# Kernel tuning notes

Hardware: AMD Instinct MI355X
Metric: run time of the kernel (lower is better)

Reference implementation:

```python
import jax, jax.numpy as jnp
import numpy as np

B, S, D = 2, 2048, 2048
H, KV, DK = 16, 4, 128
G = H // KV  # GQA groups
EPS = 1e-6
BASE = 10000.0


def _rope_tables(seq_len, dim):
    inv_freq = 1.0 / (BASE ** (jnp.arange(0, dim, 2, dtype=jnp.float32) / dim))
    t = jnp.arange(seq_len, dtype=jnp.float32)
    freqs = t[:, None] * inv_freq[None, :]            # [S, dim/2]
    emb = jnp.concatenate([freqs, freqs], axis=-1)    # [S, dim]
    # broadcast over [b, s, h, d]
    return jnp.cos(emb)[None, :, None, :], jnp.sin(emb)[None, :, None, :]


def _rotate_half(x):
    x1, x2 = jnp.split(x, 2, axis=-1)
    return jnp.concatenate([-x2, x1], axis=-1)


def _rms_norm(x, w):
    return x * jax.lax.rsqrt(jnp.mean(x * x, axis=-1, keepdims=True) + EPS) * w


def setup_inputs() -> dict:
    key = jax.random.key(0)
    ks = jax.random.split(key, 5)
    std = 0.02
    return {
        "x": jax.random.normal(ks[0], (B, S, D), jnp.float32),
        "Wq": jax.random.normal(ks[1], (D, H * DK), jnp.float32) * std,
        "Wk": jax.random.normal(ks[2], (D, KV * DK), jnp.float32) * std,
        "Wv": jax.random.normal(ks[3], (D, KV * DK), jnp.float32) * std,
        "Wo": jax.random.normal(ks[4], (H * DK, D), jnp.float32) * std,
        "q_norm_w": jnp.ones((DK,), jnp.float32),
        "k_norm_w": jnp.ones((DK,), jnp.float32),
    }


def reference(x, Wq, Wk, Wv, Wo, q_norm_w, k_norm_w):
    b, s, d = x.shape
    q = (x @ Wq).reshape(b, s, H, DK)
    k = (x @ Wk).reshape(b, s, KV, DK)
    v = (x @ Wv).reshape(b, s, KV, DK)

    # per-head RMSNorm on q/k
    q = _rms_norm(q, q_norm_w)
    k = _rms_norm(k, k_norm_w)

    # RoPE (applied in [b, s, h, d] layout like the original)
    cos, sin = _rope_tables(s, DK)
    q = q * cos + _rotate_half(q) * sin
    k = k * cos + _rotate_half(k) * sin

    # GQA attention without materializing repeated K/V:
    # q: [b, kv, g, s, d];  k, v: [b, kv, s, d]
    q = q.transpose(0, 2, 1, 3).reshape(b, KV, G, s, DK)
    k = k.transpose(0, 2, 1, 3)
    v = v.transpose(0, 2, 1, 3)

    scale = 1.0 / np.sqrt(DK)
    scores = jnp.einsum('bkgqd,bkpd->bkgqp', q, k) * scale  # [b,kv,g,s,s]
    causal = jnp.tril(jnp.ones((s, s), dtype=bool))
    scores = jnp.where(causal, scores, jnp.finfo(scores.dtype).min)
    attn = jax.nn.softmax(scores, axis=-1)
    out = jnp.einsum('bkgqp,bkpd->bkgqd', attn, v)           # [b,kv,g,s,d]

    out = out.reshape(b, H, s, DK).transpose(0, 2, 1, 3).reshape(b, s, H * DK)
    return out @ Wo
```

## Files before the change

### kernel.cpp

```cpp
#include <hip/hip_runtime.h>

typedef __attribute__((ext_vector_type(4))) float f32x4;
typedef __attribute__((ext_vector_type(8))) short s16x8;

struct alignas(8) us4 { ushort x, y, z, w; };

__device__ __forceinline__ ushort f2bf(float f) {
  unsigned u = __builtin_bit_cast(unsigned, f);
  u += 0x7fffu + ((u >> 16) & 1u);
  return (ushort)(u >> 16);
}
__device__ __forceinline__ float bf2f(ushort h) {
  unsigned u = ((unsigned)h) << 16;
  return __builtin_bit_cast(float, u);
}

__device__ __forceinline__ void gload_lds16(const ushort* g, ushort* l) {
  __builtin_amdgcn_global_load_lds((const __attribute__((address_space(1))) unsigned int*)g,
                                   (__attribute__((address_space(3))) unsigned int*)l, 16, 0, 0);
}

__global__ __launch_bounds__(256) void cast_bf16_kernel(const float* __restrict__ in,
                                                        ushort* __restrict__ out, int n4) {
  int i = blockIdx.x * 256 + threadIdx.x;
  int stride = gridDim.x * 256;
  for (; i < n4; i += stride) {
    float4 v = reinterpret_cast<const float4*>(in)[i];
    us4 o;
    o.x = f2bf(v.x); o.y = f2bf(v.y); o.z = f2bf(v.z); o.w = f2bf(v.w);
    reinterpret_cast<us4*>(out)[i] = o;
  }
}

__global__ __launch_bounds__(256) void cast_transpose_kernel(const float* __restrict__ in,
                                                             ushort* __restrict__ out,
                                                             int R, int C) {
  __shared__ float tile[32][33];
  int tx = threadIdx.x & 31, ty = threadIdx.x >> 5;
  int c0 = blockIdx.x * 32, r0 = blockIdx.y * 32;
#pragma unroll
  for (int i = 0; i < 4; ++i)
    tile[ty + i * 8][tx] = in[(size_t)(r0 + ty + i * 8) * C + c0 + tx];
  __syncthreads();
#pragma unroll
  for (int i = 0; i < 4; ++i)
    out[(size_t)(c0 + ty + i * 8) * R + r0 + tx] = f2bf(tile[tx][ty + i * 8]);
}

__global__ void rope_table_kernel(float* __restrict__ rc, float* __restrict__ rs) {
  int t = blockIdx.x, j = threadIdx.x;
  float inv = expf(-(float)j * (9.210340371976184f / 64.0f));
  float ang = (float)t * inv;
  float s, c;
  sincosf(ang, &s, &c);
  rc[t * 64 + j] = c;
  rs[t * 64 + j] = s;
}

__global__ __launch_bounds__(256) void norm_rope_kernel(
    const ushort* __restrict__ qkv, const float* __restrict__ w,
    ushort* __restrict__ out, const float* __restrict__ rc, const float* __restrict__ rs,
    int nheads, int col_off, int out_stride, float oscale) {
  int wv = threadIdx.x >> 6, lane = threadIdx.x & 63;
  int row = blockIdx.x * 4 + wv;
  int token = row / nheads, head = row % nheads;
  int t = token & 2047;
  const ushort* p = qkv + (size_t)token * 3072 + col_off + head * 128;
  float x1 = bf2f(p[lane]), x2 = bf2f(p[lane + 64]);
  float ss = x1 * x1 + x2 * x2;
#pragma unroll
  for (int m = 32; m > 0; m >>= 1) ss += __shfl_xor(ss, m);
  float r = rsqrtf(ss * (1.0f / 128.0f) + 1e-6f);
  float xn1 = x1 * r * w[lane], xn2 = x2 * r * w[lane + 64];
  float c = rc[t * 64 + lane], s = rs[t * 64 + lane];
  ushort* o = out + (size_t)token * out_stride + head * 128;
  o[lane] = f2bf((xn1 * c - xn2 * s) * oscale);
  o[lane + 64] = f2bf((xn2 * c + xn1 * s) * oscale);
}

__global__ __launch_bounds__(256) void v_transpose_kernel(const ushort* __restrict__ qkv,
                                                          ushort* __restrict__ vt) {
  __shared__ ushort tile[64][136];
  int bx = blockIdx.x;
  int st = bx & 31, kvh = (bx >> 5) & 3, b = bx >> 7;
  int s0 = st * 64;
  int tid = threadIdx.x;
#pragma unroll
  for (int p = 0; p < 4; ++p) {
    int idx = p * 2048 + tid * 8;
    int s = idx >> 7, d = idx & 127;
    *(s16x8*)&tile[s][d] =
        *(const s16x8*)&qkv[(size_t)(b * 2048 + s0 + s) * 3072 + 2560 + kvh * 128 + d];
  }
  __syncthreads();
#pragma unroll
  for (int p = 0; p < 4; ++p) {
    int idx = p * 2048 + tid * 8;
    int d = idx >> 6, s = idx & 63;
    s16x8 v;
#pragma unroll
    for (int u = 0; u < 8; ++u) v[u] = (short)tile[s + u][d];
    *(s16x8*)&vt[(size_t)((b * 4 + kvh) * 128 + d) * 2048 + s0 + s] = v;
  }
}

template <bool OUTF32>
__global__ __launch_bounds__(512, 2) void gemm256_kernel(const ushort* __restrict__ A,
                                                         const ushort* __restrict__ Bt,
                                                         void* __restrict__ Cp,
                                                         int M, int N, int K) {
  __shared__ ushort As[3][256][64];
  __shared__ ushort Bs[3][128][64];
  int tid = threadIdx.x;
  int lane = tid & 63, wv = tid >> 6;
  int wm = wv >> 1, wn = wv & 1;
  int lr = lane & 15, lg = lane >> 4;
  int nwg = gridDim.x * gridDim.y;
  int flat = blockIdx.y * gridDim.x + blockIdx.x;
  int swz = (flat & 7) * (nwg >> 3) + (flat >> 3);
  int bx = swz % gridDim.x, by = swz / gridDim.x;
  int m0 = by * 256, n0 = bx * 128;
  int srow8 = lane >> 3;
  int gcol = ((lane & 7) * 8) ^ (srow8 << 3);
  int nt = K >> 6;

  const ushort* Abase = A + (size_t)m0 * K;
  const ushort* Bbase = Bt + (size_t)n0 * K;

  auto stageA = [&](int slot, int t, int p) {
    int r0 = (wv * 4 + p) * 8;
    gload_lds16(&Abase[(size_t)(r0 + srow8) * K + t * 64 + gcol], &As[slot][r0][0]);
  };
  auto stageB = [&](int slot, int t, int p) {
    int r0 = (wv * 2 + p) * 8;
    gload_lds16(&Bbase[(size_t)(r0 + srow8) * K + t * 64 + gcol], &Bs[slot][r0][0]);
  };

  stageA(0, 0, 0); stageA(0, 0, 1); stageB(0, 0, 0);
  stageA(0, 0, 2); stageA(0, 0, 3); stageB(0, 0, 1);
  stageA(1, 1, 0); stageA(1, 1, 1); stageB(1, 1, 0);
  stageA(1, 1, 2); stageA(1, 1, 3); stageB(1, 1, 1);

  f32x4 acc[4][4] = {};
  int arow[4], brow[4], aswz[4], bswz[4];
#pragma unroll
  for (int i = 0; i < 4; ++i) {
    arow[i] = wm * 64 + i * 16 + lr;
    aswz[i] = (arow[i] & 7) << 3;
    brow[i] = wn * 64 + i * 16 + lr;
    bswz[i] = (brow[i] & 7) << 3;
  }

  for (int t = 0; t < nt; ++t) {
    int cur = t % 3, pf = (t + 2) % 3;
    if (t + 1 < nt) {
      asm volatile("s_waitcnt vmcnt(6)" ::: "memory");
    } else {
      asm volatile("s_waitcnt vmcnt(0)" ::: "memory");
    }
    __builtin_amdgcn_s_barrier();
    bool do_pf = (t + 2) < nt;
    {
      s16x8 a[4], b[4];
#pragma unroll
      for (int i = 0; i < 4; ++i) a[i] = *(const s16x8*)&As[cur][arow[i]][(lg * 8) ^ aswz[i]];
#pragma unroll
      for (int j = 0; j < 4; ++j) b[j] = *(const s16x8*)&Bs[cur][brow[j]][(lg * 8) ^ bswz[j]];
      if (do_pf) { stageA(pf, t + 2, 0); stageA(pf, t + 2, 1); stageB(pf, t + 2, 0); }
      __builtin_amdgcn_s_setprio(1);
#pragma unroll
      for (int i = 0; i < 4; ++i)
#pragma unroll
        for (int j = 0; j < 4; ++j)
          acc[i][j] = __builtin_amdgcn_mfma_f32_16x16x32_bf16(a[i], b[j], acc[i][j], 0, 0, 0);
      __builtin_amdgcn_s_setprio(0);
    }
    {
      s16x8 a[4], b[4];
#pragma unroll
      for (int i = 0; i < 4; ++i) a[i] = *(const s16x8*)&As[cur][arow[i]][(32 + lg * 8) ^ aswz[i]];
#pragma unroll
      for (int j = 0; j < 4; ++j) b[j] = *(const s16x8*)&Bs[cur][brow[j]][(32 + lg * 8) ^ bswz[j]];
      if (do_pf) { stageA(pf, t + 2, 2); stageA(pf, t + 2, 3); stageB(pf, t + 2, 1); }
      __builtin_amdgcn_s_setprio(1);
#pragma unroll
      for (int i = 0; i < 4; ++i)
#pragma unroll
        for (int j = 0; j < 4; ++j)
          acc[i][j] = __builtin_amdgcn_mfma_f32_16x16x32_bf16(a[i], b[j], acc[i][j], 0, 0, 0);
      __builtin_amdgcn_s_setprio(0);
    }
  }
#pragma unroll
  for (int i = 0; i < 4; ++i)
#pragma unroll
    for (int j = 0; j < 4; ++j) {
      int row = m0 + wm * 64 + i * 16 + lg * 4;
      int col = n0 + wn * 64 + j * 16 + lr;
#pragma unroll
      for (int r = 0; r < 4; ++r) {
        float v = acc[i][j][r];
        if (OUTF32)
          reinterpret_cast<float*>(Cp)[(size_t)(row + r) * N + col] = v;
        else
          reinterpret_cast<ushort*>(Cp)[(size_t)(row + r) * N + col] = f2bf(v);
      }
    }
}

__global__ __launch_bounds__(256, 2) void attn_kernel(const ushort* __restrict__ Q,
                                                      const ushort* __restrict__ Kn,
                                                      const ushort* __restrict__ Vt,
                                                      ushort* __restrict__ AO) {
  __shared__ ushort Ks[2][64][128];
  __shared__ ushort Vs[2][128][64];
  __shared__ ushort Ps[4][32][64];
  int bx = blockIdx.x;
  int g = bx >> 5, bh = bx & 31;
  int qt = (g < 8) ? (15 - g) : (g - 8);
  int b = bh >> 4, h = bh & 15, kvh = h >> 2;
  int q0 = qt * 128;
  int nt = 2 * qt + 2;
  int tid = threadIdx.x, lane = tid & 63, w = tid >> 6;
  int lr = lane & 15, lg = lane >> 4;

  int ksrow = lane >> 4;
  int kscol = (lane & 15) * 8;
  int vsrow = lane >> 3;
  int vscol = (lane & 7) * 8;

  auto stage = [&](int c, int t) {
    int p0 = t * 64;
#pragma unroll
    for (int p = 0; p < 4; ++p) {
      int r0 = w * 16 + p * 4;
      int row = r0 + ksrow;
      int gc = kscol ^ ((row & 7) << 3);
      gload_lds16(&Kn[(size_t)(b * 2048 + p0 + row) * 512 + kvh * 128 + gc], &Ks[c][r0][0]);
    }
#pragma unroll
    for (int p = 0; p < 4; ++p) {
      int r0 = w * 32 + p * 8;
      int row = r0 + vsrow;
      int gc = vscol ^ ((row & 7) << 3);
      gload_lds16(&Vt[(size_t)((b * 4 + kvh) * 128 + row) * 2048 + p0 + gc], &Vs[c][r0][0]);
    }
  };

  stage(0, 0);

  s16x8 qf[2][4];
#pragma unroll
  for (int qa = 0; qa < 2; ++qa) {
    const ushort* qp = &Q[(size_t)(b * 2048 + q0 + w * 32 + qa * 16 + lr) * 2048 + h * 128];
#pragma unroll
    for (int ks = 0; ks < 4; ++ks) qf[qa][ks] = *(const s16x8*)&qp[ks * 32 + lg * 8];
  }

  f32x4 O[2][8] = {};
  float mrow[2] = {-1e30f, -1e30f};
  float lrow[2] = {0.f, 0.f};

  for (int t = 0; t < nt; ++t) {
    int c = t & 1;
    if (t + 1 < nt) {
      stage(c ^ 1, t + 1);
      asm volatile("s_waitcnt vmcnt(8)" ::: "memory");
    } else {
      asm volatile("s_waitcnt vmcnt(0)" ::: "memory");
    }
    __builtin_amdgcn_s_barrier();

    bool skip = (t == 2 * qt + 1) && (w < 2);
    if (!skip) {
      f32x4 sacc[2][4] = {};
      __builtin_amdgcn_s_setprio(1);
#pragma unroll
      for (int ks = 0; ks < 4; ++ks) {
        s16x8 bk[4];
#pragma unroll
        for (int fp = 0; fp < 4; ++fp) {
          int kr = fp * 16 + lr;
          bk[fp] = *(const s16x8*)&Ks[c][kr][(ks * 32 + lg * 8) ^ ((kr & 7) << 3)];
        }
#pragma unroll
        for (int qa = 0; qa < 2; ++qa)
#pragma unroll
          for (int fp = 0; fp < 4; ++fp)
            sacc[qa][fp] = __builtin_amdgcn_mfma_f32_16x16x32_bf16(bk[fp], qf[qa][ks], sacc[qa][fp], 0, 0, 0);
      }
      __builtin_amdgcn_s_setprio(0);

      if (t >= 2 * qt) {
        int p0 = t * 64;
#pragma unroll
        for (int qa = 0; qa < 2; ++qa)
#pragma unroll
          for (int fp = 0; fp < 4; ++fp)
#pragma unroll
            for (int r = 0; r < 4; ++r) {
              int qg = q0 + w * 32 + qa * 16 + lr;
              int pg = p0 + fp * 16 + lg * 4 + r;
              if (pg > qg) sacc[qa][fp][r] = -1e30f;
            }
      }

      float pm[2];
#pragma unroll
      for (int qa = 0; qa < 2; ++qa) {
        float m01 = fmaxf(fmaxf(sacc[qa][0][0], sacc[qa][0][1]), fmaxf(sacc[qa][0][2], sacc[qa][0][3]));
#pragma unroll
        for (int fp = 1; fp < 4; ++fp)
          m01 = fmaxf(m01, fmaxf(fmaxf(sacc[qa][fp][0], sacc[qa][fp][1]),
                                 fmaxf(sacc[qa][fp][2], sacc[qa][fp][3])));
        m01 = fmaxf(m01, __shfl_xor(m01, 16));
        m01 = fmaxf(m01, __shfl_xor(m01, 32));
        pm[qa] = m01;
      }
      bool need = (pm[0] > mrow[0] + 8.0f) | (pm[1] > mrow[1] + 8.0f);
      if (__any((int)need)) {
        float fsc[2];
#pragma unroll
        for (int qa = 0; qa < 2; ++qa) {
          float mn = fmaxf(mrow[qa], pm[qa]);
          fsc[qa] = __builtin_amdgcn_exp2f(mrow[qa] - mn);
          mrow[qa] = mn;
          lrow[qa] *= fsc[qa];
        }
#pragma unroll
        for (int qa = 0; qa < 2; ++qa) {
          float fo[4];
#pragma unroll
          for (int r = 0; r < 4; ++r) fo[r] = __shfl(fsc[qa], lg * 4 + r);
#pragma unroll
          for (int fn = 0; fn < 8; ++fn)
#pragma unroll
            for (int r = 0; r < 4; ++r) O[qa][fn][r] *= fo[r];
        }
      }
      float ls[2] = {0.f, 0.f};
#pragma unroll
      for (int qa = 0; qa < 2; ++qa) {
        int prow = qa * 16 + lr;
        int swz = (lr & 7) << 3;
#pragma unroll
        for (int fp = 0; fp < 4; ++fp) {
          float e0 = __builtin_amdgcn_exp2f(sacc[qa][fp][0] - mrow[qa]);
          float e1 = __builtin_amdgcn_exp2f(sacc[qa][fp][1] - mrow[qa]);
          float e2 = __builtin_amdgcn_exp2f(sacc[qa][fp][2] - mrow[qa]);
          float e3 = __builtin_amdgcn_exp2f(sacc[qa][fp][3] - mrow[qa]);
          ls[qa] += (e0 + e1) + (e2 + e3);
          unsigned lo = (unsigned)f2bf(e0) | ((unsigned)f2bf(e1) << 16);
          unsigned hi = (unsigned)f2bf(e2) | ((unsigned)f2bf(e3) << 16);
          uint2 pk; pk.x = lo; pk.y = hi;
          *reinterpret_cast<uint2*>(&Ps[w][prow][(fp * 16 + lg * 4) ^ swz]) = pk;
        }
        ls[qa] += __shfl_xor(ls[qa], 16);
        ls[qa] += __shfl_xor(ls[qa], 32);
        lrow[qa] += ls[qa];
      }
      __builtin_amdgcn_s_setprio(1);
#pragma unroll
      for (int ks2 = 0; ks2 < 2; ++ks2) {
        s16x8 ap[2];
#pragma unroll
        for (int qa = 0; qa < 2; ++qa) {
          int prow = qa * 16 + lr;
          ap[qa] = *(const s16x8*)&Ps[w][prow][(ks2 * 32 + lg * 8) ^ ((lr & 7) << 3)];
        }
#pragma unroll
        for (int fn = 0; fn < 8; ++fn) {
          int vrow = fn * 16 + lr;
          s16x8 bv = *(const s16x8*)&Vs[c][vrow][(ks2 * 32 + lg * 8) ^ ((vrow & 7) << 3)];
#pragma unroll
          for (int qa = 0; qa < 2; ++qa)
            O[qa][fn] = __builtin_amdgcn_mfma_f32_16x16x32_bf16(ap[qa], bv, O[qa][fn], 0, 0, 0);
        }
      }
      __builtin_amdgcn_s_setprio(0);
    }
    __builtin_amdgcn_s_barrier();
  }

#pragma unroll
  for (int qa = 0; qa < 2; ++qa) {
    float inv = 1.0f / lrow[qa];
    float invq[4];
#pragma unroll
    for (int r = 0; r < 4; ++r) invq[r] = __shfl(inv, lg * 4 + r);
#pragma unroll
    for (int fn = 0; fn < 8; ++fn)
#pragma unroll
      for (int r = 0; r < 4; ++r) {
        size_t idx = (size_t)(b * 2048 + q0 + w * 32 + qa * 16 + lg * 4 + r) * 2048 +
                     h * 128 + fn * 16 + lr;
        AO[idx] = f2bf(O[qa][fn][r] * invq[r]);
      }
  }
}

extern "C" void kernel_launch(void* const* d_in, const int* in_sizes, int n_in,
                              void* d_out, int out_size, void* d_ws, size_t ws_size,
                              hipStream_t stream) {
  (void)in_sizes; (void)n_in; (void)out_size; (void)ws_size;
  const float* x = (const float*)d_in[0];
  const float* Wq = (const float*)d_in[1];
  const float* Wk = (const float*)d_in[2];
  const float* Wv = (const float*)d_in[3];
  const float* Wo = (const float*)d_in[4];
  const float* qw = (const float*)d_in[5];
  const float* kw = (const float*)d_in[6];
  float* out = (float*)d_out;

  char* ws = (char*)d_ws;
  size_t off = 0;
  auto alloc = [&](size_t bytes) {
    void* p = ws + off;
    off += (bytes + 255) & ~(size_t)255;
    return p;
  };
  ushort* xb = (ushort*)alloc((size_t)4096 * 2048 * 2);
  ushort* WqkvT = (ushort*)alloc((size_t)3072 * 2048 * 2);
  ushort* WoT = (ushort*)alloc((size_t)2048 * 2048 * 2);
  ushort* QKVraw = (ushort*)alloc((size_t)4096 * 3072 * 2);
  ushort* Qn = (ushort*)alloc((size_t)4096 * 2048 * 2);
  ushort* Kb = (ushort*)alloc((size_t)4096 * 512 * 2);
  ushort* Vt = (ushort*)alloc((size_t)4096 * 512 * 2);
  ushort* AO = (ushort*)alloc((size_t)4096 * 2048 * 2);
  float* rc = (float*)alloc((size_t)2048 * 64 * 4);
  float* rs = (float*)alloc((size_t)2048 * 64 * 4);

  const float QSCALE = 0.12751744f;

  cast_bf16_kernel<<<2048, 256, 0, stream>>>(x, xb, 4096 * 2048 / 4);
  cast_transpose_kernel<<<dim3(64, 64), 256, 0, stream>>>(Wq, WqkvT, 2048, 2048);
  cast_transpose_kernel<<<dim3(16, 64), 256, 0, stream>>>(Wk, WqkvT + (size_t)2048 * 2048, 2048, 512);
  cast_transpose_kernel<<<dim3(16, 64), 256, 0, stream>>>(Wv, WqkvT + (size_t)2560 * 2048, 2048, 512);
  cast_transpose_kernel<<<dim3(64, 64), 256, 0, stream>>>(Wo, WoT, 2048, 2048);
  rope_table_kernel<<<2048, 64, 0, stream>>>(rc, rs);
  gemm256_kernel<false><<<dim3(24, 16), 512, 0, stream>>>(xb, WqkvT, QKVraw, 4096, 3072, 2048);
  norm_rope_kernel<<<16384, 256, 0, stream>>>(QKVraw, qw, Qn, rc, rs, 16, 0, 2048, QSCALE);
  norm_rope_kernel<<<4096, 256, 0, stream>>>(QKVraw, kw, Kb, rc, rs, 4, 2048, 512, 1.0f);
  v_transpose_kernel<<<256, 256, 0, stream>>>(QKVraw, Vt);
  attn_kernel<<<512, 256, 0, stream>>>(Qn, Kb, Vt, AO);
  gemm256_kernel<true><<<dim3(16, 16), 512, 0, stream>>>(AO, WoT, out, 4096, 2048, 2048);
}
```

Measured before the change: 222.2 us.

## Fuse Q norm/RoPE into attention, software-pipeline QK^T, merge weight transposes

Q RMSNorm, RoPE and scaling now happen inside the attention kernel, which reads raw QKV directly, so the separate Q norm kernel and its Qn buffer go away. The attention loop is restructured to compute the next tile's QK^T while the current tile's softmax runs, using a triple-buffered K ring, a single-buffered V and two score accumulators swapped by an unrolled macro. The four weight cast-transpose launches are merged into one z-indexed launch. This cuts Q-tensor traffic and launch overhead and aims to hide the softmax latency, at the cost of more registers, an extra barrier per tile and the skip for the half-masked diagonal tile being dropped.

```diff
diff --git a/kernel.cpp b/kernel.cpp
--- a/kernel.cpp
+++ b/kernel.cpp
@@ -32,19 +32,31 @@
   }
 }
 
-__global__ __launch_bounds__(256) void cast_transpose_kernel(const float* __restrict__ in,
-                                                             ushort* __restrict__ out,
-                                                             int R, int C) {
+__global__ __launch_bounds__(256) void wtrans_kernel(const float* __restrict__ Wq,
+                                                     const float* __restrict__ Wk,
+                                                     const float* __restrict__ Wv,
+                                                     const float* __restrict__ Wo,
+                                                     ushort* __restrict__ WqkvT,
+                                                     ushort* __restrict__ WoT) {
   __shared__ float tile[32][33];
+  int z = blockIdx.z;
+  const float* src;
+  ushort* dst;
+  int C;
+  if (z == 0) { src = Wq; dst = WqkvT; C = 2048; }
+  else if (z == 1) { src = Wk; dst = WqkvT + (size_t)2048 * 2048; C = 512; }
+  else if (z == 2) { src = Wv; dst = WqkvT + (size_t)2560 * 2048; C = 512; }
+  else { src = Wo; dst = WoT; C = 2048; }
+  int c0 = blockIdx.x * 32, r0 = blockIdx.y * 32;
+  if (c0 >= C) return;
   int tx = threadIdx.x & 31, ty = threadIdx.x >> 5;
-  int c0 = blockIdx.x * 32, r0 = blockIdx.y * 32;
 #pragma unroll
   for (int i = 0; i < 4; ++i)
-    tile[ty + i * 8][tx] = in[(size_t)(r0 + ty + i * 8) * C + c0 + tx];
+    tile[ty + i * 8][tx] = src[(size_t)(r0 + ty + i * 8) * C + c0 + tx];
   __syncthreads();
 #pragma unroll
   for (int i = 0; i < 4; ++i)
-    out[(size_t)(c0 + ty + i * 8) * R + r0 + tx] = f2bf(tile[tx][ty + i * 8]);
+    dst[(size_t)(c0 + ty + i * 8) * 2048 + r0 + tx] = f2bf(tile[tx][ty + i * 8]);
 }
 
 __global__ void rope_table_kernel(float* __restrict__ rc, float* __restrict__ rs) {
@@ -208,15 +220,18 @@
     }
 }
 
-__global__ __launch_bounds__(256, 2) void attn_kernel(const ushort* __restrict__ Q,
+__global__ __launch_bounds__(256, 2) void attn_kernel(const ushort* __restrict__ QKV,
                                                       const ushort* __restrict__ Kn,
                                                       const ushort* __restrict__ Vt,
-                                                      ushort* __restrict__ AO) {
-  __shared__ ushort Ks[2][64][128];
-  __shared__ ushort Vs[2][128][64];
+                                                      ushort* __restrict__ AO,
+                                                      const float* __restrict__ rc,
+                                                      const float* __restrict__ rs,
+                                                      const float* __restrict__ qw) {
+  __shared__ ushort Ks[3][64][128];
+  __shared__ ushort Vs[128][64];
   __shared__ ushort Ps[4][32][64];
-  int bx = blockIdx.x;
-  int g = bx >> 5, bh = bx & 31;
+  int bxi = blockIdx.x;
+  int g = bxi >> 5, bh = bxi & 31;
   int qt = (g < 8) ? (15 - g) : (g - 8);
   int b = bh >> 4, h = bh & 15, kvh = h >> 2;
   int q0 = qt * 128;
@@ -224,163 +239,213 @@
   int tid = threadIdx.x, lane = tid & 63, w = tid >> 6;
   int lr = lane & 15, lg = lane >> 4;
 
-  int ksrow = lane >> 4;
-  int kscol = (lane & 15) * 8;
-  int vsrow = lane >> 3;
-  int vscol = (lane & 7) * 8;
-
-  auto stage = [&](int c, int t) {
+  int ksrow = lane >> 4, kscol = (lane & 15) * 8;
+  int vsrow = lane >> 3, vscol = (lane & 7) * 8;
+
+  const float QSCALE = 0.12751744f;
+  s16x8 qf[2][4];
+#pragma unroll
+  for (int qa = 0; qa < 2; ++qa) {
+    int t_tok = q0 + w * 32 + qa * 16 + lr;
+    const ushort* qp = QKV + (size_t)(b * 2048 + t_tok) * 3072 + h * 128;
+    float xv[4][8];
+    float ss = 0.f;
+#pragma unroll
+    for (int ks = 0; ks < 4; ++ks) {
+      s16x8 raw = *(const s16x8*)&qp[ks * 32 + lg * 8];
+#pragma unroll
+      for (int j = 0; j < 8; ++j) {
+        float x = bf2f((ushort)raw[j]);
+        xv[ks][j] = x;
+        ss += x * x;
+      }
+    }
+    ss += __shfl_xor(ss, 16);
+    ss += __shfl_xor(ss, 32);
+    float rms = rsqrtf(ss * (1.0f / 128.0f) + 1e-6f);
+#pragma unroll
+    for (int ks = 0; ks < 2; ++ks) {
+      int dbase = ks * 32 + lg * 8;
+      float cc[8], sn[8], w1[8], w2[8];
+      *(float4*)&cc[0] = *(const float4*)&rc[(size_t)t_tok * 64 + dbase];
+      *(float4*)&cc[4] = *(const float4*)&rc[(size_t)t_tok * 64 + dbase + 4];
+      *(float4*)&sn[0] = *(const float4*)&rs[(size_t)t_tok * 64 + dbase];
+      *(float4*)&sn[4] = *(const float4*)&rs[(size_t)t_tok * 64 + dbase + 4];
+      *(float4*)&w1[0] = *(const float4*)&qw[dbase];
+      *(float4*)&w1[4] = *(const float4*)&qw[dbase + 4];
+      *(float4*)&w2[0] = *(const float4*)&qw[dbase + 64];
+      *(float4*)&w2[4] = *(const float4*)&qw[dbase + 68];
+      s16x8 o1, o2;
+#pragma unroll
+      for (int j = 0; j < 8; ++j) {
+        float x1 = xv[ks][j] * rms * w1[j];
+        float x2 = xv[ks + 2][j] * rms * w2[j];
+        o1[j] = (short)f2bf((x1 * cc[j] - x2 * sn[j]) * QSCALE);
+        o2[j] = (short)f2bf((x2 * cc[j] + x1 * sn[j]) * QSCALE);
+      }
+      qf[qa][ks] = o1;
+      qf[qa][ks + 2] = o2;
+    }
+  }
+  asm volatile("s_waitcnt vmcnt(0)" ::: "memory");
+
+  auto stageK = [&](int slot, int t) {
     int p0 = t * 64;
 #pragma unroll
     for (int p = 0; p < 4; ++p) {
       int r0 = w * 16 + p * 4;
       int row = r0 + ksrow;
       int gc = kscol ^ ((row & 7) << 3);
-      gload_lds16(&Kn[(size_t)(b * 2048 + p0 + row) * 512 + kvh * 128 + gc], &Ks[c][r0][0]);
-    }
+      gload_lds16(&Kn[(size_t)(b * 2048 + p0 + row) * 512 + kvh * 128 + gc], &Ks[slot][r0][0]);
+    }
+  };
+  auto stageV = [&](int t) {
+    int p0 = t * 64;
 #pragma unroll
     for (int p = 0; p < 4; ++p) {
       int r0 = w * 32 + p * 8;
       int row = r0 + vsrow;
       int gc = vscol ^ ((row & 7) << 3);
-      gload_lds16(&Vt[(size_t)((b * 4 + kvh) * 128 + row) * 2048 + p0 + gc], &Vs[c][r0][0]);
+      gload_lds16(&Vt[(size_t)((b * 4 + kvh) * 128 + row) * 2048 + p0 + gc], &Vs[r0][0]);
     }
   };
 
-  stage(0, 0);
-
-  s16x8 qf[2][4];
-#pragma unroll
-  for (int qa = 0; qa < 2; ++qa) {
-    const ushort* qp = &Q[(size_t)(b * 2048 + q0 + w * 32 + qa * 16 + lr) * 2048 + h * 128];
-#pragma unroll
-    for (int ks = 0; ks < 4; ++ks) qf[qa][ks] = *(const s16x8*)&qp[ks * 32 + lg * 8];
-  }
+  stageK(0, 0);
+  stageK(1, 1);
+  asm volatile("s_waitcnt vmcnt(4)" ::: "memory");
+  __builtin_amdgcn_s_barrier();
+
+  f32x4 sacc0[2][4] = {}, sacc1[2][4];
+  __builtin_amdgcn_s_setprio(1);
+#pragma unroll
+  for (int ks = 0; ks < 4; ++ks) {
+    s16x8 bk[4];
+#pragma unroll
+    for (int fp = 0; fp < 4; ++fp) {
+      int kr = fp * 16 + lr;
+      bk[fp] = *(const s16x8*)&Ks[0][kr][(ks * 32 + lg * 8) ^ ((kr & 7) << 3)];
+    }
+#pragma unroll
+    for (int qa = 0; qa < 2; ++qa)
+#pragma unroll
+      for (int fp = 0; fp < 4; ++fp)
+        sacc0[qa][fp] = __builtin_amdgcn_mfma_f32_16x16x32_bf16(bk[fp], qf[qa][ks], sacc0[qa][fp], 0, 0, 0);
+  }
+  __builtin_amdgcn_s_setprio(0);
 
   f32x4 O[2][8] = {};
-  float mrow[2] = {-1e30f, -1e30f};
-  float lrow[2] = {0.f, 0.f};
-
-  for (int t = 0; t < nt; ++t) {
-    int c = t & 1;
-    if (t + 1 < nt) {
-      stage(c ^ 1, t + 1);
-      asm volatile("s_waitcnt vmcnt(8)" ::: "memory");
-    } else {
-      asm volatile("s_waitcnt vmcnt(0)" ::: "memory");
-    }
-    __builtin_amdgcn_s_barrier();
-
-    bool skip = (t == 2 * qt + 1) && (w < 2);
-    if (!skip) {
-      f32x4 sacc[2][4] = {};
-      __builtin_amdgcn_s_setprio(1);
-#pragma unroll
-      for (int ks = 0; ks < 4; ++ks) {
-        s16x8 bk[4];
-#pragma unroll
-        for (int fp = 0; fp < 4; ++fp) {
-          int kr = fp * 16 + lr;
-          bk[fp] = *(const s16x8*)&Ks[c][kr][(ks * 32 + lg * 8) ^ ((kr & 7) << 3)];
-        }
-#pragma unroll
-        for (int qa = 0; qa < 2; ++qa)
-#pragma unroll
-          for (int fp = 0; fp < 4; ++fp)
-            sacc[qa][fp] = __builtin_amdgcn_mfma_f32_16x16x32_bf16(bk[fp], qf[qa][ks], sacc[qa][fp], 0, 0, 0);
-      }
-      __builtin_amdgcn_s_setprio(0);
-
-      if (t >= 2 * qt) {
-        int p0 = t * 64;
-#pragma unroll
-        for (int qa = 0; qa < 2; ++qa)
-#pragma unroll
-          for (int fp = 0; fp < 4; ++fp)
-#pragma unroll
-            for (int r = 0; r < 4; ++r) {
-              int qg = q0 + w * 32 + qa * 16 + lr;
-              int pg = p0 + fp * 16 + lg * 4 + r;
-              if (pg > qg) sacc[qa][fp][r] = -1e30f;
-            }
-      }
-
-      float pm[2];
-#pragma unroll
-      for (int qa = 0; qa < 2; ++qa) {
-        float m01 = fmaxf(fmaxf(sacc[qa][0][0], sacc[qa][0][1]), fmaxf(sacc[qa][0][2], sacc[qa][0][3]));
-#pragma unroll
-        for (int fp = 1; fp < 4; ++fp)
-          m01 = fmaxf(m01, fmaxf(fmaxf(sacc[qa][fp][0], sacc[qa][fp][1]),
-                                 fmaxf(sacc[qa][fp][2], sacc[qa][fp][3])));
-        m01 = fmaxf(m01, __shfl_xor(m01, 16));
-        m01 = fmaxf(m01, __shfl_xor(m01, 32));
-        pm[qa] = m01;
-      }
-      bool need = (pm[0] > mrow[0] + 8.0f) | (pm[1] > mrow[1] + 8.0f);
-      if (__any((int)need)) {
-        float fsc[2];
-#pragma unroll
-        for (int qa = 0; qa < 2; ++qa) {
-          float mn = fmaxf(mrow[qa], pm[qa]);
-          fsc[qa] = __builtin_amdgcn_exp2f(mrow[qa] - mn);
-          mrow[qa] = mn;
-          lrow[qa] *= fsc[qa];
-        }
-#pragma unroll
-        for (int qa = 0; qa < 2; ++qa) {
-          float fo[4];
-#pragma unroll
-          for (int r = 0; r < 4; ++r) fo[r] = __shfl(fsc[qa], lg * 4 + r);
-#pragma unroll
-          for (int fn = 0; fn < 8; ++fn)
-#pragma unroll
-            for (int r = 0; r < 4; ++r) O[qa][fn][r] *= fo[r];
-        }
-      }
-      float ls[2] = {0.f, 0.f};
-#pragma unroll
-      for (int qa = 0; qa < 2; ++qa) {
-        int prow = qa * 16 + lr;
-        int swz = (lr & 7) << 3;
-#pragma unroll
-        for (int fp = 0; fp < 4; ++fp) {
-          float e0 = __builtin_amdgcn_exp2f(sacc[qa][fp][0] - mrow[qa]);
-          float e1 = __builtin_amdgcn_exp2f(sacc[qa][fp][1] - mrow[qa]);
-          float e2 = __builtin_amdgcn_exp2f(sacc[qa][fp][2] - mrow[qa]);
-          float e3 = __builtin_amdgcn_exp2f(sacc[qa][fp][3] - mrow[qa]);
-          ls[qa] += (e0 + e1) + (e2 + e3);
-          unsigned lo = (unsigned)f2bf(e0) | ((unsigned)f2bf(e1) << 16);
-          unsigned hi = (unsigned)f2bf(e2) | ((unsigned)f2bf(e3) << 16);
-          uint2 pk; pk.x = lo; pk.y = hi;
-          *reinterpret_cast<uint2*>(&Ps[w][prow][(fp * 16 + lg * 4) ^ swz]) = pk;
-        }
-        ls[qa] += __shfl_xor(ls[qa], 16);
-        ls[qa] += __shfl_xor(ls[qa], 32);
-        lrow[qa] += ls[qa];
-      }
-      __builtin_amdgcn_s_setprio(1);
-#pragma unroll
-      for (int ks2 = 0; ks2 < 2; ++ks2) {
-        s16x8 ap[2];
-#pragma unroll
-        for (int qa = 0; qa < 2; ++qa) {
-          int prow = qa * 16 + lr;
-          ap[qa] = *(const s16x8*)&Ps[w][prow][(ks2 * 32 + lg * 8) ^ ((lr & 7) << 3)];
-        }
-#pragma unroll
-        for (int fn = 0; fn < 8; ++fn) {
-          int vrow = fn * 16 + lr;
-          s16x8 bv = *(const s16x8*)&Vs[c][vrow][(ks2 * 32 + lg * 8) ^ ((vrow & 7) << 3)];
-#pragma unroll
-          for (int qa = 0; qa < 2; ++qa)
-            O[qa][fn] = __builtin_amdgcn_mfma_f32_16x16x32_bf16(ap[qa], bv, O[qa][fn], 0, 0, 0);
-        }
-      }
-      __builtin_amdgcn_s_setprio(0);
-    }
-    __builtin_amdgcn_s_barrier();
-  }
+  float mrow[2] = {-1e30f, -1e30f}, lrow[2] = {0.f, 0.f};
+
+#define ATTN_ITER(T, CUR, NXT)                                                        \
+  {                                                                                   \
+    const int t_ = (T);                                                               \
+    asm volatile("s_waitcnt vmcnt(0)" ::: "memory");                                  \
+    __builtin_amdgcn_s_barrier();                                                     \
+    stageV(t_);                                                                       \
+    const bool pfK_ = (t_ + 2) < nt;                                                  \
+    if (pfK_) stageK((t_ + 2) % 3, t_ + 2);                                           \
+    if (t_ + 1 < nt) {                                                                \
+      int sl_ = (t_ + 1) % 3;                                                         \
+      _Pragma("unroll") for (int qa = 0; qa < 2; ++qa)                                \
+          _Pragma("unroll") for (int fp = 0; fp < 4; ++fp)                            \
+              NXT[qa][fp] = (f32x4){0.f, 0.f, 0.f, 0.f};                              \
+      __builtin_amdgcn_s_setprio(1);                                                  \
+      _Pragma("unroll") for (int ks = 0; ks < 4; ++ks) {                              \
+        s16x8 bk[4];                                                                  \
+        _Pragma("unroll") for (int fp = 0; fp < 4; ++fp) {                            \
+          int kr = fp * 16 + lr;                                                      \
+          bk[fp] = *(const s16x8*)&Ks[sl_][kr][(ks * 32 + lg * 8) ^ ((kr & 7) << 3)]; \
+        }                                                                             \
+        _Pragma("unroll") for (int qa = 0; qa < 2; ++qa)                              \
+            _Pragma("unroll") for (int fp = 0; fp < 4; ++fp)                          \
+                NXT[qa][fp] = __builtin_amdgcn_mfma_f32_16x16x32_bf16(                \
+                    bk[fp], qf[qa][ks], NXT[qa][fp], 0, 0, 0);                        \
+      }                                                                               \
+      __builtin_amdgcn_s_setprio(0);                                                  \
+    }                                                                                 \
+    if (t_ >= 2 * qt) {                                                               \
+      int p0_ = t_ * 64;                                                              \
+      _Pragma("unroll") for (int qa = 0; qa < 2; ++qa)                                \
+          _Pragma("unroll") for (int fp = 0; fp < 4; ++fp)                            \
+              _Pragma("unroll") for (int r = 0; r < 4; ++r) {                         \
+        int qg = q0 + w * 32 + qa * 16 + lr;                                          \
+        int pg = p0_ + fp * 16 + lg * 4 + r;                                          \
+        if (pg > qg) CUR[qa][fp][r] = -1e30f;                                         \
+      }                                                                               \
+    }                                                                                 \
+    float pm_[2];                                                                     \
+    _Pragma("unroll") for (int qa = 0; qa < 2; ++qa) {                                \
+      float m01 = fmaxf(fmaxf(CUR[qa][0][0], CUR[qa][0][1]),                          \
+                        fmaxf(CUR[qa][0][2], CUR[qa][0][3]));                         \
+      _Pragma("unroll") for (int fp = 1; fp < 4; ++fp)                                \
+          m01 = fmaxf(m01, fmaxf(fmaxf(CUR[qa][fp][0], CUR[qa][fp][1]),               \
+                                 fmaxf(CUR[qa][fp][2], CUR[qa][fp][3])));             \
+      m01 = fmaxf(m01, __shfl_xor(m01, 16));                                          \
+      m01 = fmaxf(m01, __shfl_xor(m01, 32));                                          \
+      pm_[qa] = m01;                                                                  \
+    }                                                                                 \
+    bool need_ = (pm_[0] > mrow[0] + 8.0f) | (pm_[1] > mrow[1] + 8.0f);               \
+    if (__any((int)need_)) {                                                          \
+      float fsc_[2];                                                                  \
+      _Pragma("unroll") for (int qa = 0; qa < 2; ++qa) {                              \
+        float mn = fmaxf(mrow[qa], pm_[qa]);                                          \
+        fsc_[qa] = __builtin_amdgcn_exp2f(mrow[qa] - mn);                             \
+        mrow[qa] = mn;                                                                \
+        lrow[qa] *= fsc_[qa];                                                         \
+      }                                                                               \
+      _Pragma("unroll") for (int qa = 0; qa < 2; ++qa) {                              \
+        float fo_[4];                                                                 \
+        _Pragma("unroll") for (int r = 0; r < 4; ++r)                                 \
+            fo_[r] = __shfl(fsc_[qa], lg * 4 + r);                                    \
+        _Pragma("unroll") for (int fn = 0; fn < 8; ++fn)                              \
+            _Pragma("unroll") for (int r = 0; r < 4; ++r) O[qa][fn][r] *= fo_[r];     \
+      }                                                                               \
+    }                                                                                 \
+    _Pragma("unroll") for (int qa = 0; qa < 2; ++qa) {                                \
+      float ls_ = 0.f;                                                                \
+      int prow = qa * 16 + lr;                                                        \
+      int swz_ = (lr & 7) << 3;                                                       \
+      _Pragma("unroll") for (int fp = 0; fp < 4; ++fp) {                              \
+        float e0 = __builtin_amdgcn_exp2f(CUR[qa][fp][0] - mrow[qa]);                 \
+        float e1 = __builtin_amdgcn_exp2f(CUR[qa][fp][1] - mrow[qa]);                 \
+        float e2 = __builtin_amdgcn_exp2f(CUR[qa][fp][2] - mrow[qa]);                 \
+        float e3 = __builtin_amdgcn_exp2f(CUR[qa][fp][3] - mrow[qa]);                 \
+        ls_ += (e0 + e1) + (e2 + e3);                                                 \
+        unsigned lo = (unsigned)f2bf(e0) | ((unsigned)f2bf(e1) << 16);                \
+        unsigned hi = (unsigned)f2bf(e2) | ((unsigned)f2bf(e3) << 16);                \
+        uint2 pk; pk.x = lo; pk.y = hi;                                               \
+        *reinterpret_cast<uint2*>(&Ps[w][prow][(fp * 16 + lg * 4) ^ swz_]) = pk;      \
+      }                                                                               \
+      ls_ += __shfl_xor(ls_, 16);                                                     \
+      ls_ += __shfl_xor(ls_, 32);                                                     \
+      lrow[qa] += ls_;                                                                \
+    }                                                                                 \
+    if (pfK_) { asm volatile("s_waitcnt vmcnt(4)" ::: "memory"); }                    \
+    else      { asm volatile("s_waitcnt vmcnt(0)" ::: "memory"); }                    \
+    __builtin_amdgcn_s_barrier();                                                     \
+    __builtin_amdgcn_s_setprio(1);                                                    \
+    _Pragma("unroll") for (int ks2 = 0; ks2 < 2; ++ks2) {                             \
+      s16x8 ap[2];                                                                    \
+      _Pragma("unroll") for (int qa = 0; qa < 2; ++qa) {                              \
+        int prow = qa * 16 + lr;                                                      \
+        ap[qa] = *(const s16x8*)&Ps[w][prow][(ks2 * 32 + lg * 8) ^ ((lr & 7) << 3)];  \
+      }                                                                               \
+      _Pragma("unroll") for (int fn = 0; fn < 8; ++fn) {                              \
+        int vrow = fn * 16 + lr;                                                      \
+        s16x8 bv = *(const s16x8*)&Vs[vrow][(ks2 * 32 + lg * 8) ^ ((vrow & 7) << 3)]; \
+        _Pragma("unroll") for (int qa = 0; qa < 2; ++qa)                              \
+            O[qa][fn] = __builtin_amdgcn_mfma_f32_16x16x32_bf16(ap[qa], bv,           \
+                                                                O[qa][fn], 0, 0, 0);  \
+      }                                                                               \
+    }                                                                                 \
+    __builtin_amdgcn_s_setprio(0);                                                    \
+  }
+
+  for (int t = 0; t < nt; t += 2) {
+    ATTN_ITER(t, sacc0, sacc1);
+    ATTN_ITER(t + 1, sacc1, sacc0);
+  }
+#undef ATTN_ITER
 
 #pragma unroll
   for (int qa = 0; qa < 2; ++qa) {
@@ -423,25 +488,18 @@
   ushort* WqkvT = (ushort*)alloc((size_t)3072 * 2048 * 2);
   ushort* WoT = (ushort*)alloc((size_t)2048 * 2048 * 2);
   ushort* QKVraw = (ushort*)alloc((size_t)4096 * 3072 * 2);
-  ushort* Qn = (ushort*)alloc((size_t)4096 * 2048 * 2);
   ushort* Kb = (ushort*)alloc((size_t)4096 * 512 * 2);
   ushort* Vt = (ushort*)alloc((size_t)4096 * 512 * 2);
   ushort* AO = (ushort*)alloc((size_t)4096 * 2048 * 2);
   float* rc = (float*)alloc((size_t)2048 * 64 * 4);
   float* rs = (float*)alloc((size_t)2048 * 64 * 4);
 
-  const float QSCALE = 0.12751744f;
-
   cast_bf16_kernel<<<2048, 256, 0, stream>>>(x, xb, 4096 * 2048 / 4);
-  cast_transpose_kernel<<<dim3(64, 64), 256, 0, stream>>>(Wq, WqkvT, 2048, 2048);
-  cast_transpose_kernel<<<dim3(16, 64), 256, 0, stream>>>(Wk, WqkvT + (size_t)2048 * 2048, 2048, 512);
-  cast_transpose_kernel<<<dim3(16, 64), 256, 0, stream>>>(Wv, WqkvT + (size_t)2560 * 2048, 2048, 512);
-  cast_transpose_kernel<<<dim3(64, 64), 256, 0, stream>>>(Wo, WoT, 2048, 2048);
+  wtrans_kernel<<<dim3(64, 64, 4), 256, 0, stream>>>(Wq, Wk, Wv, Wo, WqkvT, WoT);
   rope_table_kernel<<<2048, 64, 0, stream>>>(rc, rs);
   gemm256_kernel<false><<<dim3(24, 16), 512, 0, stream>>>(xb, WqkvT, QKVraw, 4096, 3072, 2048);
-  norm_rope_kernel<<<16384, 256, 0, stream>>>(QKVraw, qw, Qn, rc, rs, 16, 0, 2048, QSCALE);
   norm_rope_kernel<<<4096, 256, 0, stream>>>(QKVraw, kw, Kb, rc, rs, 4, 2048, 512, 1.0f);
   v_transpose_kernel<<<256, 256, 0, stream>>>(QKVraw, Vt);
-  attn_kernel<<<512, 256, 0, stream>>>(Qn, Kb, Vt, AO);
+  attn_kernel<<<512, 256, 0, stream>>>(QKVraw, Kb, Vt, AO, rc, rs, qw);
   gemm256_kernel<true><<<dim3(16, 16), 512, 0, stream>>>(AO, WoT, out, 4096, 2048, 2048);
 }
```

Result: faster. 209.6 us (-5.7%).

## Fuse Q RMSNorm+RoPE into attention prologue and merge weight transposes

Applied to the files above, without the earlier changes.

The Q-side RMSNorm, RoPE and scaling are moved into the attention kernel's Q fragment load, reading raw QKV directly. This removes the separate norm_rope launch for Q and its 16 MB bf16 write and read-back. The four weight cast-transpose launches are also merged into one 3D-grid launch, with early exit for out-of-range blocks. Each attention block now redoes the norm math for its Q rows and adds register pressure in the prologue, and the K staging now starts only after the Q prologue.

```diff
diff --git a/kernel.cpp b/kernel.cpp
--- a/kernel.cpp
+++ b/kernel.cpp
@@ -32,19 +32,31 @@
   }
 }
 
-__global__ __launch_bounds__(256) void cast_transpose_kernel(const float* __restrict__ in,
-                                                             ushort* __restrict__ out,
-                                                             int R, int C) {
+__global__ __launch_bounds__(256) void wtrans_kernel(const float* __restrict__ Wq,
+                                                     const float* __restrict__ Wk,
+                                                     const float* __restrict__ Wv,
+                                                     const float* __restrict__ Wo,
+                                                     ushort* __restrict__ WqkvT,
+                                                     ushort* __restrict__ WoT) {
   __shared__ float tile[32][33];
+  int z = blockIdx.z;
+  const float* src;
+  ushort* dst;
+  int C;
+  if (z == 0) { src = Wq; dst = WqkvT; C = 2048; }
+  else if (z == 1) { src = Wk; dst = WqkvT + (size_t)2048 * 2048; C = 512; }
+  else if (z == 2) { src = Wv; dst = WqkvT + (size_t)2560 * 2048; C = 512; }
+  else { src = Wo; dst = WoT; C = 2048; }
+  int c0 = blockIdx.x * 32, r0 = blockIdx.y * 32;
+  if (c0 >= C) return;
   int tx = threadIdx.x & 31, ty = threadIdx.x >> 5;
-  int c0 = blockIdx.x * 32, r0 = blockIdx.y * 32;
 #pragma unroll
   for (int i = 0; i < 4; ++i)
-    tile[ty + i * 8][tx] = in[(size_t)(r0 + ty + i * 8) * C + c0 + tx];
+    tile[ty + i * 8][tx] = src[(size_t)(r0 + ty + i * 8) * C + c0 + tx];
   __syncthreads();
 #pragma unroll
   for (int i = 0; i < 4; ++i)
-    out[(size_t)(c0 + ty + i * 8) * R + r0 + tx] = f2bf(tile[tx][ty + i * 8]);
+    dst[(size_t)(c0 + ty + i * 8) * 2048 + r0 + tx] = f2bf(tile[tx][ty + i * 8]);
 }
 
 __global__ void rope_table_kernel(float* __restrict__ rc, float* __restrict__ rs) {
@@ -208,15 +220,18 @@
     }
 }
 
-__global__ __launch_bounds__(256, 2) void attn_kernel(const ushort* __restrict__ Q,
+__global__ __launch_bounds__(256, 2) void attn_kernel(const ushort* __restrict__ QKV,
                                                       const ushort* __restrict__ Kn,
                                                       const ushort* __restrict__ Vt,
-                                                      ushort* __restrict__ AO) {
+                                                      ushort* __restrict__ AO,
+                                                      const float* __restrict__ rc,
+                                                      const float* __restrict__ rs,
+                                                      const float* __restrict__ qw) {
   __shared__ ushort Ks[2][64][128];
   __shared__ ushort Vs[2][128][64];
   __shared__ ushort Ps[4][32][64];
-  int bx = blockIdx.x;
-  int g = bx >> 5, bh = bx & 31;
+  int bxi = blockIdx.x;
+  int g = bxi >> 5, bh = bxi & 31;
   int qt = (g < 8) ? (15 - g) : (g - 8);
   int b = bh >> 4, h = bh & 15, kvh = h >> 2;
   int q0 = qt * 128;
@@ -224,10 +239,55 @@
   int tid = threadIdx.x, lane = tid & 63, w = tid >> 6;
   int lr = lane & 15, lg = lane >> 4;
 
-  int ksrow = lane >> 4;
-  int kscol = (lane & 15) * 8;
-  int vsrow = lane >> 3;
-  int vscol = (lane & 7) * 8;
+  int ksrow = lane >> 4, kscol = (lane & 15) * 8;
+  int vsrow = lane >> 3, vscol = (lane & 7) * 8;
+
+  const float QSCALE = 0.12751744f;
+  s16x8 qf[2][4];
+#pragma unroll
+  for (int qa = 0; qa < 2; ++qa) {
+    int t_tok = q0 + w * 32 + qa * 16 + lr;
+    const ushort* qp = QKV + (size_t)(b * 2048 + t_tok) * 3072 + h * 128;
+    float xv[4][8];
+    float ss = 0.f;
+#pragma unroll
+    for (int ks = 0; ks < 4; ++ks) {
+      s16x8 raw = *(const s16x8*)&qp[ks * 32 + lg * 8];
+#pragma unroll
+      for (int j = 0; j < 8; ++j) {
+        float x = bf2f((ushort)raw[j]);
+        xv[ks][j] = x;
+        ss += x * x;
+      }
+    }
+    ss += __shfl_xor(ss, 16);
+    ss += __shfl_xor(ss, 32);
+    float rms = rsqrtf(ss * (1.0f / 128.0f) + 1e-6f);
+#pragma unroll
+    for (int ks = 0; ks < 2; ++ks) {
+      int dbase = ks * 32 + lg * 8;
+      float cc[8], sn[8], w1[8], w2[8];
+      *(float4*)&cc[0] = *(const float4*)&rc[(size_t)t_tok * 64 + dbase];
+      *(float4*)&cc[4] = *(const float4*)&rc[(size_t)t_tok * 64 + dbase + 4];
+      *(float4*)&sn[0] = *(const float4*)&rs[(size_t)t_tok * 64 + dbase];
+      *(float4*)&sn[4] = *(const float4*)&rs[(size_t)t_tok * 64 + dbase + 4];
+      *(float4*)&w1[0] = *(const float4*)&qw[dbase];
+      *(float4*)&w1[4] = *(const float4*)&qw[dbase + 4];
+      *(float4*)&w2[0] = *(const float4*)&qw[dbase + 64];
+      *(float4*)&w2[4] = *(const float4*)&qw[dbase + 68];
+      s16x8 o1, o2;
+#pragma unroll
+      for (int j = 0; j < 8; ++j) {
+        float x1 = xv[ks][j] * rms * w1[j];
+        float x2 = xv[ks + 2][j] * rms * w2[j];
+        o1[j] = (short)f2bf((x1 * cc[j] - x2 * sn[j]) * QSCALE);
+        o2[j] = (short)f2bf((x2 * cc[j] + x1 * sn[j]) * QSCALE);
+      }
+      qf[qa][ks] = o1;
+      qf[qa][ks + 2] = o2;
+    }
+  }
+  asm volatile("s_waitcnt vmcnt(0)" ::: "memory");
 
   auto stage = [&](int c, int t) {
     int p0 = t * 64;
@@ -248,14 +308,6 @@
   };
 
   stage(0, 0);
-
-  s16x8 qf[2][4];
-#pragma unroll
-  for (int qa = 0; qa < 2; ++qa) {
-    const ushort* qp = &Q[(size_t)(b * 2048 + q0 + w * 32 + qa * 16 + lr) * 2048 + h * 128];
-#pragma unroll
-    for (int ks = 0; ks < 4; ++ks) qf[qa][ks] = *(const s16x8*)&qp[ks * 32 + lg * 8];
-  }
 
   f32x4 O[2][8] = {};
   float mrow[2] = {-1e30f, -1e30f};
@@ -423,25 +475,18 @@
   ushort* WqkvT = (ushort*)alloc((size_t)3072 * 2048 * 2);
   ushort* WoT = (ushort*)alloc((size_t)2048 * 2048 * 2);
   ushort* QKVraw = (ushort*)alloc((size_t)4096 * 3072 * 2);
-  ushort* Qn = (ushort*)alloc((size_t)4096 * 2048 * 2);
   ushort* Kb = (ushort*)alloc((size_t)4096 * 512 * 2);
   ushort* Vt = (ushort*)alloc((size_t)4096 * 512 * 2);
   ushort* AO = (ushort*)alloc((size_t)4096 * 2048 * 2);
   float* rc = (float*)alloc((size_t)2048 * 64 * 4);
   float* rs = (float*)alloc((size_t)2048 * 64 * 4);
 
-  const float QSCALE = 0.12751744f;
-
   cast_bf16_kernel<<<2048, 256, 0, stream>>>(x, xb, 4096 * 2048 / 4);
-  cast_transpose_kernel<<<dim3(64, 64), 256, 0, stream>>>(Wq, WqkvT, 2048, 2048);
-  cast_transpose_kernel<<<dim3(16, 64), 256, 0, stream>>>(Wk, WqkvT + (size_t)2048 * 2048, 2048, 512);
-  cast_transpose_kernel<<<dim3(16, 64), 256, 0, stream>>>(Wv, WqkvT + (size_t)2560 * 2048, 2048, 512);
-  cast_transpose_kernel<<<dim3(64, 64), 256, 0, stream>>>(Wo, WoT, 2048, 2048);
+  wtrans_kernel<<<dim3(64, 64, 4), 256, 0, stream>>>(Wq, Wk, Wv, Wo, WqkvT, WoT);
   rope_table_kernel<<<2048, 64, 0, stream>>>(rc, rs);
   gemm256_kernel<false><<<dim3(24, 16), 512, 0, stream>>>(xb, WqkvT, QKVraw, 4096, 3072, 2048);
-  norm_rope_kernel<<<16384, 256, 0, stream>>>(QKVraw, qw, Qn, rc, rs, 16, 0, 2048, QSCALE);
   norm_rope_kernel<<<4096, 256, 0, stream>>>(QKVraw, kw, Kb, rc, rs, 4, 2048, 512, 1.0f);
   v_transpose_kernel<<<256, 256, 0, stream>>>(QKVraw, Vt);
-  attn_kernel<<<512, 256, 0, stream>>>(Qn, Kb, Vt, AO);
+  attn_kernel<<<512, 256, 0, stream>>>(QKVraw, Kb, Vt, AO, rc, rs, qw);
   gemm256_kernel<true><<<dim3(16, 16), 512, 0, stream>>>(AO, WoT, out, 4096, 2048, 2048);
 }
```

After: 208.7 us. 6.1% less time.
